# Kernel optimization log

Measured on AMD Instinct MI355X. Metric: run time of the kernel, lower is better.

The kernel has to match this reference:

```python
import jax, jax.numpy as jnp
import numpy as np
from jax import lax

# ---- geometry constants ----
H = W = 128            # image shape
A = 96                 # num angles
D = 128                # detector count
T = 182                # ray integration steps (~128*sqrt(2))
N_ITER = 10
OP_NORM = 128.0

_angles = np.linspace(0.0, np.pi, A, endpoint=False).astype(np.float32)
COS = jnp.asarray(np.cos(_angles))
SIN = jnp.asarray(np.sin(_angles))


def _bilinear(img, xi, yi):
    # img: [B,H,W]; xi,yi: [A,D,T] pixel coords -> [B,A,D,T]
    x0 = jnp.floor(xi)
    y0 = jnp.floor(yi)
    wx = xi - x0
    wy = yi - y0
    x0i = x0.astype(jnp.int32)
    y0i = y0.astype(jnp.int32)
    x1i = x0i + 1
    y1i = y0i + 1

    def g(yy, xx):
        valid = ((xx >= 0) & (xx < W) & (yy >= 0) & (yy < H)).astype(img.dtype)
        v = img[:, jnp.clip(yy, 0, H - 1), jnp.clip(xx, 0, W - 1)]
        return v * valid[None]

    return (g(y0i, x0i) * ((1 - wy) * (1 - wx))[None]
            + g(y0i, x1i) * ((1 - wy) * wx)[None]
            + g(y1i, x0i) * (wy * (1 - wx))[None]
            + g(y1i, x1i) * (wy * wx)[None])


def radon_fwd(x):
    # x: [B,H,W,1] -> sinogram [B,A,D,1]
    img = x[..., 0]
    s = (jnp.arange(D, dtype=jnp.float32) - (D - 1) / 2)[None, :, None]   # [1,D,1]
    t = (jnp.arange(T, dtype=jnp.float32) - (T - 1) / 2)[None, None, :]   # [1,1,T]
    c = COS[:, None, None]
    sn = SIN[:, None, None]
    px = s * c - t * sn            # [A,D,T] world coords
    py = s * sn + t * c
    xi = px + (W - 1) / 2
    yi = py + (H - 1) / 2
    sino = _bilinear(img, xi, yi).sum(axis=-1)   # [B,A,D]
    return sino[..., None]


def radon_adj(sino):
    # sino: [B,A,D,1] -> backprojection [B,H,W,1]
    s = sino[..., 0]   # [B,A,D]
    px = jnp.arange(W, dtype=jnp.float32) - (W - 1) / 2
    py = jnp.arange(H, dtype=jnp.float32) - (H - 1) / 2
    det = (px[None, None, :] * COS[:, None, None]
           + py[None, :, None] * SIN[:, None, None] + (D - 1) / 2)  # [A,H,W]
    d0f = jnp.floor(det)
    w = det - d0f
    d0 = d0f.astype(jnp.int32)
    d1 = d0 + 1
    aidx = jnp.arange(A)[:, None, None]

    def g(dd):
        valid = ((dd >= 0) & (dd < D)).astype(s.dtype)
        return s[:, aidx, jnp.clip(dd, 0, D - 1)] * valid[None]

    out = (g(d0) * (1 - w)[None] + g(d1) * w[None]).sum(axis=1)  # [B,H,W]
    return out[..., None]


def _conv(x, w, b):
    return lax.conv_general_dilated(x, w, (1, 1), 'SAME',
                                    dimension_numbers=('NHWC', 'HWIO', 'NHWC')) + b


def _block(x, w1, b1, w2, b2, w3, b3):
    x = jax.nn.relu(_conv(x, w1, b1))
    x = jax.nn.relu(_conv(x, w2, b2))
    return _conv(x, w3, b3)


def setup_inputs() -> dict:
    key = jax.random.key(0)
    ks = jax.random.split(key, 8)
    B = 4
    sc = 0.05
    return {
        'y': jax.random.normal(ks[0], (B, A, D, 1), jnp.float32),
        'sigma': jnp.full((1,), 0.5, jnp.float32),
        'tau': jnp.full((1,), 0.5, jnp.float32),
        'theta': jnp.ones((1,), jnp.float32),
        'dw1': jax.random.normal(ks[1], (3, 3, 7, 32), jnp.float32) * sc,
        'db1': jnp.zeros((32,), jnp.float32),
        'dw2': jax.random.normal(ks[2], (3, 3, 32, 32), jnp.float32) * sc,
        'db2': jnp.zeros((32,), jnp.float32),
        'dw3': jax.random.normal(ks[3], (3, 3, 32, 5), jnp.float32) * sc,
        'db3': jnp.zeros((5,), jnp.float32),
        'pw1': jax.random.normal(ks[4], (3, 3, 6, 32), jnp.float32) * sc,
        'pb1': jnp.zeros((32,), jnp.float32),
        'pw2': jax.random.normal(ks[5], (3, 3, 32, 32), jnp.float32) * sc,
        'pb2': jnp.zeros((32,), jnp.float32),
        'pw3': jax.random.normal(ks[6], (3, 3, 32, 5), jnp.float32) * sc,
        'pb3': jnp.zeros((5,), jnp.float32),
    }


def reference(y, sigma, tau, theta, dw1, db1, dw2, db2, dw3, db3,
              pw1, pb1, pw2, pb2, pw3, pb3):
    B = y.shape[0]
    n_primal, n_dual = 5, 5
    primal = jnp.zeros((B, H, W, n_primal), y.dtype)
    primal_bar = jnp.zeros((B, H, W, n_primal), y.dtype)
    dual = jnp.zeros((B, A, D, n_dual), y.dtype)

    def step(carry, _):
        primal, primal_bar, dual = carry
        evalop = radon_fwd(primal_bar[..., 1:2]) / OP_NORM
        dual_in = jnp.concatenate([dual, evalop, y], axis=-1)
        dual = dual + sigma * _block(dual_in, dw1, db1, dw2, db2, dw3, db3)
        evalop_adj = radon_adj(dual[..., 0:1]) / OP_NORM
        primal_in = jnp.concatenate([primal, evalop_adj], axis=-1)
        primal_old = primal
        primal = primal + tau * _block(primal_in, pw1, pb1, pw2, pb2, pw3, pb3)
        primal_bar = primal + theta * (primal - primal_old)
        return (primal, primal_bar, dual), None

    (primal, _, _), _ = lax.scan(step, (primal, primal_bar, dual), None, length=N_ITER)
    return primal[..., 0:1]
```

## Files before the change

### kernel.cpp

```cpp
#include <hip/hip_runtime.h>
#include <math.h>

#define BB 4
#define HHH 128
#define WWW 128
#define AANG 96
#define DDET 128
#define TSTEP 182
#define M_P (BB*HHH*WWW)
#define M_D (BB*AANG*DDET)
#define INV_OPN (1.0f/128.0f)

typedef __bf16 bf16x8 __attribute__((ext_vector_type(8)));
typedef float  f32x4  __attribute__((ext_vector_type(4)));

__device__ __forceinline__ void split_store(__bf16* hi, __bf16* lo, int off, float v) {
    __bf16 h = (__bf16)v;
    hi[off] = h;
    lo[off] = (__bf16)(v - (float)h);
}

template<int CIP, int NCH, int NCOT, int IH>
__device__ __forceinline__ void conv_core(
        const __bf16* __restrict__ Ahi, const __bf16* __restrict__ Alo,
        const __bf16* __restrict__ Whi, const __bf16* __restrict__ Wlo,
        int mtile, f32x4 acc[NCOT])
{
    const int IW = 128;
    const int COP = NCOT * 16;
    int lane = threadIdx.x & 63;
    int n16  = lane & 15;
    int quad = lane >> 4;
    int p0  = mtile * 16;
    int b   = p0 / (IH * IW);
    int rem = p0 - b * (IH * IW);
    int ty  = rem >> 7;
    int tx0 = rem & 127;
    #pragma unroll
    for (int c = 0; c < NCH; ++c) {
        int tap = (CIP == 32) ? c : (c * 4 + quad);
        int dy = tap / 3 - 1;
        int dx = tap % 3 - 1;
        int yy = ty + dy;
        int xx = tx0 + n16 + dx;
        bool valid = (tap < 9) && (yy >= 0) && (yy < IH) && (xx >= 0) && (xx < IW);
        bf16x8 a_h = {};
        bf16x8 a_l = {};
        if (valid) {
            size_t off = (size_t)(b * IH * IW + yy * IW + xx) * CIP
                       + ((CIP == 32) ? (quad * 8) : 0);
            a_h = *(const bf16x8*)(Ahi + off);
            a_l = *(const bf16x8*)(Alo + off);
        }
        #pragma unroll
        for (int ct = 0; ct < NCOT; ++ct) {
            size_t woff = ((size_t)tap * COP + ct * 16 + n16) * CIP
                        + ((CIP == 32) ? (quad * 8) : 0);
            bf16x8 b_h = *(const bf16x8*)(Whi + woff);
            bf16x8 b_l = *(const bf16x8*)(Wlo + woff);
            acc[ct] = __builtin_amdgcn_mfma_f32_16x16x32_bf16(a_h, b_h, acc[ct], 0, 0, 0);
            acc[ct] = __builtin_amdgcn_mfma_f32_16x16x32_bf16(a_h, b_l, acc[ct], 0, 0, 0);
            acc[ct] = __builtin_amdgcn_mfma_f32_16x16x32_bf16(a_l, b_h, acc[ct], 0, 0, 0);
        }
    }
}

template<int CIP, int NCH, int IH>
__global__ __launch_bounds__(256) void conv_ab_k(
        const __bf16* __restrict__ Ahi, const __bf16* __restrict__ Alo,
        const __bf16* __restrict__ Whi, const __bf16* __restrict__ Wlo,
        const float* __restrict__ bias,
        __bf16* __restrict__ Ohi, __bf16* __restrict__ Olo, int Mtiles)
{
    int wid = (blockIdx.x * 256 + threadIdx.x) >> 6;
    if (wid >= Mtiles) return;
    f32x4 acc[2] = {};
    conv_core<CIP, NCH, 2, IH>(Ahi, Alo, Whi, Wlo, wid, acc);
    int lane = threadIdx.x & 63;
    int n16 = lane & 15;
    int quad = lane >> 4;
    #pragma unroll
    for (int ct = 0; ct < 2; ++ct) {
        float bv = bias[ct * 16 + n16];
        #pragma unroll
        for (int r = 0; r < 4; ++r) {
            float v = acc[ct][r] + bv;
            v = fmaxf(v, 0.f);
            int m = wid * 16 + quad * 4 + r;
            split_store(Ohi, Olo, m * 32 + ct * 16 + n16, v);
        }
    }
}

template<int IH>
__global__ __launch_bounds__(256) void conv_c_dual_k(
        const __bf16* __restrict__ Ahi, const __bf16* __restrict__ Alo,
        const __bf16* __restrict__ Whi, const __bf16* __restrict__ Wlo,
        const float* __restrict__ bias, const float* __restrict__ sigma_p,
        float* __restrict__ dual_f, __bf16* __restrict__ cat_hi, __bf16* __restrict__ cat_lo,
        float* __restrict__ dual0, int Mtiles)
{
    int wid = (blockIdx.x * 256 + threadIdx.x) >> 6;
    if (wid >= Mtiles) return;
    f32x4 acc[1] = {};
    conv_core<32, 9, 1, IH>(Ahi, Alo, Whi, Wlo, wid, acc);
    int lane = threadIdx.x & 63;
    int n16 = lane & 15;
    int quad = lane >> 4;
    if (n16 < 5) {
        float sg = *sigma_p;
        float bv = bias[n16];
        #pragma unroll
        for (int r = 0; r < 4; ++r) {
            int m = wid * 16 + quad * 4 + r;
            float v = acc[0][r] + bv;
            float dn = dual_f[m * 5 + n16] + sg * v;
            dual_f[m * 5 + n16] = dn;
            split_store(cat_hi, cat_lo, m * 8 + n16, dn);
            if (n16 == 0) dual0[m] = dn;
        }
    }
}

template<int IH>
__global__ __launch_bounds__(256) void conv_c_prim_k(
        const __bf16* __restrict__ Ahi, const __bf16* __restrict__ Alo,
        const __bf16* __restrict__ Whi, const __bf16* __restrict__ Wlo,
        const float* __restrict__ bias, const float* __restrict__ tau_p,
        const float* __restrict__ theta_p,
        float* __restrict__ primal_f, __bf16* __restrict__ cat_hi, __bf16* __restrict__ cat_lo,
        float* __restrict__ pbar1, int Mtiles)
{
    int wid = (blockIdx.x * 256 + threadIdx.x) >> 6;
    if (wid >= Mtiles) return;
    f32x4 acc[1] = {};
    conv_core<32, 9, 1, IH>(Ahi, Alo, Whi, Wlo, wid, acc);
    int lane = threadIdx.x & 63;
    int n16 = lane & 15;
    int quad = lane >> 4;
    if (n16 < 5) {
        float ta = *tau_p;
        float th = *theta_p;
        float bv = bias[n16];
        #pragma unroll
        for (int r = 0; r < 4; ++r) {
            int m = wid * 16 + quad * 4 + r;
            float v = acc[0][r] + bv;
            float pold = primal_f[m * 5 + n16];
            float pn = pold + ta * v;
            primal_f[m * 5 + n16] = pn;
            split_store(cat_hi, cat_lo, m * 8 + n16, pn);
            if (n16 == 1) pbar1[m] = pn + th * (pn - pold);
        }
    }
}

__global__ __launch_bounds__(256) void radon_fwd_part_k(const float* __restrict__ img,
                                                        float* __restrict__ part)
{
    int idx = blockIdx.x * 256 + threadIdx.x;
    int q = idx / M_D;
    int pix = idx - q * M_D;
    int d = pix & 127;
    int b = pix / (AANG * DDET);
    int a = (pix - b * AANG * DDET) >> 7;
    float ang = (float)((double)a * M_PI / (double)AANG);
    float c = cosf(ang), sn = sinf(ang);
    float s = (float)d - 63.5f;
    float scx = s * c, ssy = s * sn;
    const float* ib = img + b * (HHH * WWW);
    float acc = 0.f;
    int t0 = q * 46;
    int t1 = t0 + 46 < TSTEP ? t0 + 46 : TSTEP;
    for (int tt = t0; tt < t1; ++tt) {
        float t = (float)tt - 90.5f;
        float xi = (scx - t * sn) + 63.5f;
        float yi = (ssy + t * c) + 63.5f;
        float x0f = floorf(xi), y0f = floorf(yi);
        float wx = xi - x0f, wy = yi - y0f;
        int x0 = (int)x0f, y0 = (int)y0f;
        int x1 = x0 + 1, y1 = y0 + 1;
        bool xv0 = (x0 >= 0) & (x0 < WWW);
        bool xv1 = (x1 >= 0) & (x1 < WWW);
        bool yv0 = (y0 >= 0) & (y0 < HHH);
        bool yv1 = (y1 >= 0) & (y1 < HHH);
        float v00 = (yv0 & xv0) ? ib[y0 * WWW + x0] : 0.f;
        float v01 = (yv0 & xv1) ? ib[y0 * WWW + x1] : 0.f;
        float v10 = (yv1 & xv0) ? ib[y1 * WWW + x0] : 0.f;
        float v11 = (yv1 & xv1) ? ib[y1 * WWW + x1] : 0.f;
        acc += v00 * (1.f - wy) * (1.f - wx) + v01 * (1.f - wy) * wx
             + v10 * wy * (1.f - wx) + v11 * wy * wx;
    }
    part[idx] = acc;
}

__global__ __launch_bounds__(256) void fwd_combine_k(const float* __restrict__ part,
                                                     __bf16* __restrict__ cat_hi,
                                                     __bf16* __restrict__ cat_lo)
{
    int pix = blockIdx.x * 256 + threadIdx.x;
    if (pix >= M_D) return;
    float v = (part[pix] + part[M_D + pix] + part[2 * M_D + pix] + part[3 * M_D + pix]) * INV_OPN;
    split_store(cat_hi, cat_lo, pix * 8 + 5, v);
}

__global__ __launch_bounds__(256) void radon_adj_part_k(const float* __restrict__ sino0,
                                                        float* __restrict__ part)
{
    __shared__ float cs[AANG], ss[AANG];
    int tid = threadIdx.x;
    if (tid < AANG) {
        double ang = (double)tid * M_PI / (double)AANG;
        cs[tid] = (float)cos(ang);
        ss[tid] = (float)sin(ang);
    }
    __syncthreads();
    int idx = blockIdx.x * 256 + tid;
    int h = idx >> 16;
    int pix = idx & (M_P - 1);
    int x = pix & 127;
    int yv = (pix >> 7) & 127;
    int b = pix >> 14;
    float px = (float)x - 63.5f;
    float py = (float)yv - 63.5f;
    const float* sb = sino0 + b * (AANG * DDET);
    float acc = 0.f;
    int a0 = h * 48;
    for (int a = a0; a < a0 + 48; ++a) {
        float det = px * cs[a] + py * ss[a] + 63.5f;
        float dh = floorf(det);
        float w = det - dh;
        int d0 = (int)dh;
        int d1 = d0 + 1;
        float v0 = (d0 >= 0 && d0 < DDET) ? sb[a * DDET + d0] : 0.f;
        float v1 = (d1 >= 0 && d1 < DDET) ? sb[a * DDET + d1] : 0.f;
        acc += v0 * (1.f - w) + v1 * w;
    }
    part[idx] = acc;
}

__global__ __launch_bounds__(256) void adj_combine_k(const float* __restrict__ part,
                                                     __bf16* __restrict__ cat_hi,
                                                     __bf16* __restrict__ cat_lo)
{
    int pix = blockIdx.x * 256 + threadIdx.x;
    if (pix >= M_P) return;
    float v = (part[pix] + part[M_P + pix]) * INV_OPN;
    split_store(cat_hi, cat_lo, pix * 8 + 5, v);
}

__global__ __launch_bounds__(256) void y_conv_k(const float* __restrict__ y,
                                                __bf16* __restrict__ cat_hi,
                                                __bf16* __restrict__ cat_lo)
{
    int pix = blockIdx.x * 256 + threadIdx.x;
    if (pix >= M_D) return;
    split_store(cat_hi, cat_lo, pix * 8 + 6, y[pix]);
}

__global__ __launch_bounds__(256) void prep_w_k(
        const float* __restrict__ dw1, const float* __restrict__ dw2, const float* __restrict__ dw3,
        const float* __restrict__ pw1, const float* __restrict__ pw2, const float* __restrict__ pw3,
        __bf16* __restrict__ wT)
{
    __bf16* d1h = wT;            __bf16* d1l = d1h + 3072;
    __bf16* d2h = d1l + 3072;    __bf16* d2l = d2h + 9216;
    __bf16* d3h = d2l + 9216;    __bf16* d3l = d3h + 4608;
    __bf16* p1h = d3l + 4608;    __bf16* p1l = p1h + 3072;
    __bf16* p2h = p1l + 3072;    __bf16* p2l = p2h + 9216;
    __bf16* p3h = p2l + 9216;    __bf16* p3l = p3h + 4608;
    int i = blockIdx.x * 256 + threadIdx.x;
    if (i < 2016) {
        int co = i & 31; int r = i >> 5; int ci = r % 7; int tap = r / 7;
        split_store(d1h, d1l, (tap * 32 + co) * 8 + ci, dw1[i]);
        return;
    }
    i -= 2016;
    if (i < 9216) {
        int co = i & 31; int r = i >> 5; int ci = r & 31; int tap = r >> 5;
        split_store(d2h, d2l, (tap * 32 + co) * 32 + ci, dw2[i]);
        return;
    }
    i -= 9216;
    if (i < 1440) {
        int co = i % 5; int r = i / 5; int ci = r & 31; int tap = r >> 5;
        split_store(d3h, d3l, (tap * 16 + co) * 32 + ci, dw3[i]);
        return;
    }
    i -= 1440;
    if (i < 1728) {
        int co = i & 31; int r = i >> 5; int ci = r % 6; int tap = r / 6;
        split_store(p1h, p1l, (tap * 32 + co) * 8 + ci, pw1[i]);
        return;
    }
    i -= 1728;
    if (i < 9216) {
        int co = i & 31; int r = i >> 5; int ci = r & 31; int tap = r >> 5;
        split_store(p2h, p2l, (tap * 32 + co) * 32 + ci, pw2[i]);
        return;
    }
    i -= 9216;
    if (i < 1440) {
        int co = i % 5; int r = i / 5; int ci = r & 31; int tap = r >> 5;
        split_store(p3h, p3l, (tap * 16 + co) * 32 + ci, pw3[i]);
        return;
    }
}

__global__ __launch_bounds__(256) void extract_k(const float* __restrict__ primal_f,
                                                 float* __restrict__ out)
{
    int pix = blockIdx.x * 256 + threadIdx.x;
    if (pix >= M_P) return;
    out[pix] = primal_f[pix * 5];
}

extern "C" void kernel_launch(void* const* d_in, const int* in_sizes, int n_in,
                              void* d_out, int out_size, void* d_ws, size_t ws_size,
                              hipStream_t stream) {
    const float* y     = (const float*)d_in[0];
    const float* sigma = (const float*)d_in[1];
    const float* tau   = (const float*)d_in[2];
    const float* theta = (const float*)d_in[3];
    const float* dw1 = (const float*)d_in[4];
    const float* db1 = (const float*)d_in[5];
    const float* dw2 = (const float*)d_in[6];
    const float* db2 = (const float*)d_in[7];
    const float* dw3 = (const float*)d_in[8];
    const float* db3 = (const float*)d_in[9];
    const float* pw1 = (const float*)d_in[10];
    const float* pb1 = (const float*)d_in[11];
    const float* pw2 = (const float*)d_in[12];
    const float* pb2 = (const float*)d_in[13];
    const float* pw3 = (const float*)d_in[14];
    const float* pb3 = (const float*)d_in[15];

    float* ws = (float*)d_ws;
    float* primal_f = ws;
    float* dual_f   = primal_f + M_P * 5;
    float* pbar1    = dual_f + M_D * 5;
    float* dual0    = pbar1 + M_P;
    float* fwd_part = dual0 + M_D;
    float* adj_part = fwd_part + 4 * M_D;
    __bf16* bf = (__bf16*)(adj_part + 2 * M_P);
    __bf16* cat_d_hi = bf;
    __bf16* cat_d_lo = cat_d_hi + M_D * 8;
    __bf16* cat_p_hi = cat_d_lo + M_D * 8;
    __bf16* cat_p_lo = cat_p_hi + M_P * 8;
    __bf16* hidA_hi  = cat_p_lo + M_P * 8;
    __bf16* hidA_lo  = hidA_hi + M_P * 32;
    __bf16* hidB_hi  = hidA_lo + M_P * 32;
    __bf16* hidB_lo  = hidB_hi + M_P * 32;
    __bf16* wT       = hidB_lo + M_P * 32;

    __bf16* d1h = wT;            __bf16* d1l = d1h + 3072;
    __bf16* d2h = d1l + 3072;    __bf16* d2l = d2h + 9216;
    __bf16* d3h = d2l + 9216;    __bf16* d3l = d3h + 4608;
    __bf16* p1h = d3l + 4608;    __bf16* p1l = p1h + 3072;
    __bf16* p2h = p1l + 3072;    __bf16* p2l = p2h + 9216;
    __bf16* p3h = p2l + 9216;    __bf16* p3l = p3h + 4608;

    hipMemsetAsync(primal_f, 0, (size_t)(M_P * 5 + M_D * 5 + M_P) * 4, stream);
    hipMemsetAsync(cat_d_hi, 0, (size_t)(M_D * 16 + M_P * 16) * 2, stream);
    hipMemsetAsync(wT, 0, (size_t)67584 * 2, stream);

    prep_w_k<<<98, 256, 0, stream>>>(dw1, dw2, dw3, pw1, pw2, pw3, wT);
    y_conv_k<<<M_D / 256, 256, 0, stream>>>(y, cat_d_hi, cat_d_lo);

    const int MT_D = M_D / 16;
    const int MT_P = M_P / 16;

    for (int it = 0; it < 10; ++it) {
        radon_fwd_part_k<<<4 * M_D / 256, 256, 0, stream>>>(pbar1, fwd_part);
        fwd_combine_k<<<M_D / 256, 256, 0, stream>>>(fwd_part, cat_d_hi, cat_d_lo);
        conv_ab_k<8, 3, AANG><<<MT_D / 4, 256, 0, stream>>>(cat_d_hi, cat_d_lo, d1h, d1l, db1, hidA_hi, hidA_lo, MT_D);
        conv_ab_k<32, 9, AANG><<<MT_D / 4, 256, 0, stream>>>(hidA_hi, hidA_lo, d2h, d2l, db2, hidB_hi, hidB_lo, MT_D);
        conv_c_dual_k<AANG><<<MT_D / 4, 256, 0, stream>>>(hidB_hi, hidB_lo, d3h, d3l, db3, sigma, dual_f, cat_d_hi, cat_d_lo, dual0, MT_D);
        radon_adj_part_k<<<2 * M_P / 256, 256, 0, stream>>>(dual0, adj_part);
        adj_combine_k<<<M_P / 256, 256, 0, stream>>>(adj_part, cat_p_hi, cat_p_lo);
        conv_ab_k<8, 3, HHH><<<MT_P / 4, 256, 0, stream>>>(cat_p_hi, cat_p_lo, p1h, p1l, pb1, hidA_hi, hidA_lo, MT_P);
        conv_ab_k<32, 9, HHH><<<MT_P / 4, 256, 0, stream>>>(hidA_hi, hidA_lo, p2h, p2l, pb2, hidB_hi, hidB_lo, MT_P);
        conv_c_prim_k<HHH><<<MT_P / 4, 256, 0, stream>>>(hidB_hi, hidB_lo, p3h, p3l, pb3, tau, theta, primal_f, cat_p_hi, cat_p_lo, pbar1, MT_P);
    }
    extract_k<<<M_P / 256, 256, 0, stream>>>(primal_f, (float*)d_out);
}
```

Measured before the change: 1.168 ms.

## Fuse radon partial sums with combine, clip ray range, precompute trig table

Result: faster. 1.087 ms (-7.0%).

```diff
diff --git a/kernel.cpp b/kernel.cpp
--- a/kernel.cpp
+++ b/kernel.cpp
@@ -155,27 +155,50 @@
     }
 }
 
-__global__ __launch_bounds__(256) void radon_fwd_part_k(const float* __restrict__ img,
-                                                        float* __restrict__ part)
-{
-    int idx = blockIdx.x * 256 + threadIdx.x;
-    int q = idx / M_D;
-    int pix = idx - q * M_D;
+__global__ __launch_bounds__(256) void radon_fwd_fused_k(const float* __restrict__ img,
+                                                         const float* __restrict__ trig,
+                                                         __bf16* __restrict__ cat_hi,
+                                                         __bf16* __restrict__ cat_lo)
+{
+    __shared__ float red[256];
+    int tid = threadIdx.x;
+    int q = tid >> 6;
+    int j = tid & 63;
+    int pix = blockIdx.x * 64 + j;
     int d = pix & 127;
     int b = pix / (AANG * DDET);
     int a = (pix - b * AANG * DDET) >> 7;
-    float ang = (float)((double)a * M_PI / (double)AANG);
-    float c = cosf(ang), sn = sinf(ang);
+    float c  = trig[a];
+    float sn = trig[AANG + a];
     float s = (float)d - 63.5f;
-    float scx = s * c, ssy = s * sn;
+    float A = s * c + 63.5f;
+    float C = s * sn + 63.5f;
+    float tlo = -1e30f, thi = 1e30f;
+    if (sn > 1e-6f) {
+        tlo = (A - 128.f) / sn;
+        thi = (A + 1.f) / sn;
+    }
+    if (c > 1e-6f) {
+        tlo = fmaxf(tlo, (-1.f - C) / c);
+        thi = fminf(thi, (128.f - C) / c);
+    } else if (c < -1e-6f) {
+        tlo = fmaxf(tlo, (128.f - C) / c);
+        thi = fminf(thi, (-1.f - C) / c);
+    }
+    float flo = fmaxf(fminf(tlo + 90.5f, 300.f), -300.f);
+    float fhi = fmaxf(fminf(thi + 90.5f, 300.f), -300.f);
+    int clo = (int)floorf(flo) - 1;
+    int chi = (int)floorf(fhi) + 2;
+    int t0 = q * 46;
+    int t1 = t0 + 46 < TSTEP ? t0 + 46 : TSTEP;
+    if (clo > t0) t0 = clo;
+    if (chi < t1) t1 = chi;
     const float* ib = img + b * (HHH * WWW);
     float acc = 0.f;
-    int t0 = q * 46;
-    int t1 = t0 + 46 < TSTEP ? t0 + 46 : TSTEP;
     for (int tt = t0; tt < t1; ++tt) {
         float t = (float)tt - 90.5f;
-        float xi = (scx - t * sn) + 63.5f;
-        float yi = (ssy + t * c) + 63.5f;
+        float xi = A - t * sn;
+        float yi = C + t * c;
         float x0f = floorf(xi), y0f = floorf(yi);
         float wx = xi - x0f, wy = yi - y0f;
         int x0 = (int)x0f, y0 = (int)y0f;
@@ -191,33 +214,31 @@
         acc += v00 * (1.f - wy) * (1.f - wx) + v01 * (1.f - wy) * wx
              + v10 * wy * (1.f - wx) + v11 * wy * wx;
     }
-    part[idx] = acc;
-}
-
-__global__ __launch_bounds__(256) void fwd_combine_k(const float* __restrict__ part,
-                                                     __bf16* __restrict__ cat_hi,
-                                                     __bf16* __restrict__ cat_lo)
-{
-    int pix = blockIdx.x * 256 + threadIdx.x;
-    if (pix >= M_D) return;
-    float v = (part[pix] + part[M_D + pix] + part[2 * M_D + pix] + part[3 * M_D + pix]) * INV_OPN;
-    split_store(cat_hi, cat_lo, pix * 8 + 5, v);
-}
-
-__global__ __launch_bounds__(256) void radon_adj_part_k(const float* __restrict__ sino0,
-                                                        float* __restrict__ part)
+    red[tid] = acc;
+    __syncthreads();
+    if (tid < 64) {
+        int p2 = blockIdx.x * 64 + tid;
+        float v = (red[tid] + red[tid + 64] + red[tid + 128] + red[tid + 192]) * INV_OPN;
+        split_store(cat_hi, cat_lo, p2 * 8 + 5, v);
+    }
+}
+
+__global__ __launch_bounds__(256) void radon_adj_fused_k(const float* __restrict__ sino0,
+                                                         const float* __restrict__ trig,
+                                                         __bf16* __restrict__ cat_hi,
+                                                         __bf16* __restrict__ cat_lo)
 {
     __shared__ float cs[AANG], ss[AANG];
+    __shared__ float red[256];
     int tid = threadIdx.x;
     if (tid < AANG) {
-        double ang = (double)tid * M_PI / (double)AANG;
-        cs[tid] = (float)cos(ang);
-        ss[tid] = (float)sin(ang);
+        cs[tid] = trig[tid];
+        ss[tid] = trig[AANG + tid];
     }
     __syncthreads();
-    int idx = blockIdx.x * 256 + tid;
-    int h = idx >> 16;
-    int pix = idx & (M_P - 1);
+    int h = tid >> 7;
+    int j = tid & 127;
+    int pix = blockIdx.x * 128 + j;
     int x = pix & 127;
     int yv = (pix >> 7) & 127;
     int b = pix >> 14;
@@ -236,32 +257,20 @@
         float v1 = (d1 >= 0 && d1 < DDET) ? sb[a * DDET + d1] : 0.f;
         acc += v0 * (1.f - w) + v1 * w;
     }
-    part[idx] = acc;
-}
-
-__global__ __launch_bounds__(256) void adj_combine_k(const float* __restrict__ part,
-                                                     __bf16* __restrict__ cat_hi,
-                                                     __bf16* __restrict__ cat_lo)
-{
-    int pix = blockIdx.x * 256 + threadIdx.x;
-    if (pix >= M_P) return;
-    float v = (part[pix] + part[M_P + pix]) * INV_OPN;
-    split_store(cat_hi, cat_lo, pix * 8 + 5, v);
-}
-
-__global__ __launch_bounds__(256) void y_conv_k(const float* __restrict__ y,
-                                                __bf16* __restrict__ cat_hi,
-                                                __bf16* __restrict__ cat_lo)
-{
-    int pix = blockIdx.x * 256 + threadIdx.x;
-    if (pix >= M_D) return;
-    split_store(cat_hi, cat_lo, pix * 8 + 6, y[pix]);
-}
-
-__global__ __launch_bounds__(256) void prep_w_k(
+    red[tid] = acc;
+    __syncthreads();
+    if (tid < 128) {
+        float v = (red[tid] + red[tid + 128]) * INV_OPN;
+        split_store(cat_hi, cat_lo, (blockIdx.x * 128 + tid) * 8 + 5, v);
+    }
+}
+
+__global__ __launch_bounds__(256) void prep_all_k(
         const float* __restrict__ dw1, const float* __restrict__ dw2, const float* __restrict__ dw3,
         const float* __restrict__ pw1, const float* __restrict__ pw2, const float* __restrict__ pw3,
-        __bf16* __restrict__ wT)
+        const float* __restrict__ y,
+        __bf16* __restrict__ wT, float* __restrict__ trig,
+        __bf16* __restrict__ cat_d_hi, __bf16* __restrict__ cat_d_lo)
 {
     __bf16* d1h = wT;            __bf16* d1l = d1h + 3072;
     __bf16* d2h = d1l + 3072;    __bf16* d2l = d2h + 9216;
@@ -270,6 +279,13 @@
     __bf16* p2h = p1l + 3072;    __bf16* p2l = p2h + 9216;
     __bf16* p3h = p2l + 9216;    __bf16* p3l = p3h + 4608;
     int i = blockIdx.x * 256 + threadIdx.x;
+    if (i < AANG) {
+        double ang = (double)i * M_PI / (double)AANG;
+        trig[i] = (float)cos(ang);
+        trig[AANG + i] = (float)sin(ang);
+        return;
+    }
+    i -= AANG;
     if (i < 2016) {
         int co = i & 31; int r = i >> 5; int ci = r % 7; int tap = r / 7;
         split_store(d1h, d1l, (tap * 32 + co) * 8 + ci, dw1[i]);
@@ -303,6 +319,11 @@
     if (i < 1440) {
         int co = i % 5; int r = i / 5; int ci = r & 31; int tap = r >> 5;
         split_store(p3h, p3l, (tap * 16 + co) * 32 + ci, pw3[i]);
+        return;
+    }
+    i -= 1440;
+    if (i < M_D) {
+        split_store(cat_d_hi, cat_d_lo, i * 8 + 6, y[i]);
         return;
     }
 }
@@ -339,19 +360,18 @@
     float* primal_f = ws;
     float* dual_f   = primal_f + M_P * 5;
     float* pbar1    = dual_f + M_D * 5;
-    float* dual0    = pbar1 + M_P;
-    float* fwd_part = dual0 + M_D;
-    float* adj_part = fwd_part + 4 * M_D;
-    __bf16* bf = (__bf16*)(adj_part + 2 * M_P);
+    __bf16* bf = (__bf16*)(pbar1 + M_P);
     __bf16* cat_d_hi = bf;
     __bf16* cat_d_lo = cat_d_hi + M_D * 8;
     __bf16* cat_p_hi = cat_d_lo + M_D * 8;
     __bf16* cat_p_lo = cat_p_hi + M_P * 8;
-    __bf16* hidA_hi  = cat_p_lo + M_P * 8;
-    __bf16* hidA_lo  = hidA_hi + M_P * 32;
-    __bf16* hidB_hi  = hidA_lo + M_P * 32;
-    __bf16* hidB_lo  = hidB_hi + M_P * 32;
-    __bf16* wT       = hidB_lo + M_P * 32;
+    __bf16* wT       = cat_p_lo + M_P * 8;
+    float* trig     = (float*)(wT + 67584);
+    float* dual0    = trig + 192;
+    __bf16* hidA_hi = (__bf16*)(dual0 + M_D);
+    __bf16* hidA_lo = hidA_hi + M_P * 32;
+    __bf16* hidB_hi = hidA_lo + M_P * 32;
+    __bf16* hidB_lo = hidB_hi + M_P * 32;
 
     __bf16* d1h = wT;            __bf16* d1l = d1h + 3072;
     __bf16* d2h = d1l + 3072;    __bf16* d2l = d2h + 9216;
@@ -360,24 +380,25 @@
     __bf16* p2h = p1l + 3072;    __bf16* p2l = p2h + 9216;
     __bf16* p3h = p2l + 9216;    __bf16* p3l = p3h + 4608;
 
-    hipMemsetAsync(primal_f, 0, (size_t)(M_P * 5 + M_D * 5 + M_P) * 4, stream);
-    hipMemsetAsync(cat_d_hi, 0, (size_t)(M_D * 16 + M_P * 16) * 2, stream);
-    hipMemsetAsync(wT, 0, (size_t)67584 * 2, stream);
-
-    prep_w_k<<<98, 256, 0, stream>>>(dw1, dw2, dw3, pw1, pw2, pw3, wT);
-    y_conv_k<<<M_D / 256, 256, 0, stream>>>(y, cat_d_hi, cat_d_lo);
+    size_t zbytes = (size_t)(M_P * 5 + M_D * 5 + M_P) * 4
+                  + (size_t)(M_D * 16 + M_P * 16 + 67584) * 2;
+    hipMemsetAsync(ws, 0, zbytes, stream);
+
+    {
+        int items = AANG + 25056 + M_D;
+        prep_all_k<<<(items + 255) / 256, 256, 0, stream>>>(dw1, dw2, dw3, pw1, pw2, pw3, y,
+                                                            wT, trig, cat_d_hi, cat_d_lo);
+    }
 
     const int MT_D = M_D / 16;
     const int MT_P = M_P / 16;
 
     for (int it = 0; it < 10; ++it) {
-        radon_fwd_part_k<<<4 * M_D / 256, 256, 0, stream>>>(pbar1, fwd_part);
-        fwd_combine_k<<<M_D / 256, 256, 0, stream>>>(fwd_part, cat_d_hi, cat_d_lo);
+        radon_fwd_fused_k<<<M_D / 64, 256, 0, stream>>>(pbar1, trig, cat_d_hi, cat_d_lo);
         conv_ab_k<8, 3, AANG><<<MT_D / 4, 256, 0, stream>>>(cat_d_hi, cat_d_lo, d1h, d1l, db1, hidA_hi, hidA_lo, MT_D);
         conv_ab_k<32, 9, AANG><<<MT_D / 4, 256, 0, stream>>>(hidA_hi, hidA_lo, d2h, d2l, db2, hidB_hi, hidB_lo, MT_D);
         conv_c_dual_k<AANG><<<MT_D / 4, 256, 0, stream>>>(hidB_hi, hidB_lo, d3h, d3l, db3, sigma, dual_f, cat_d_hi, cat_d_lo, dual0, MT_D);
-        radon_adj_part_k<<<2 * M_P / 256, 256, 0, stream>>>(dual0, adj_part);
-        adj_combine_k<<<M_P / 256, 256, 0, stream>>>(adj_part, cat_p_hi, cat_p_lo);
+        radon_adj_fused_k<<<M_P / 128, 256, 0, stream>>>(dual0, trig, cat_p_hi, cat_p_lo);
         conv_ab_k<8, 3, HHH><<<MT_P / 4, 256, 0, stream>>>(cat_p_hi, cat_p_lo, p1h, p1l, pb1, hidA_hi, hidA_lo, MT_P);
         conv_ab_k<32, 9, HHH><<<MT_P / 4, 256, 0, stream>>>(hidA_hi, hidA_lo, p2h, p2l, pb2, hidB_hi, hidB_lo, MT_P);
         conv_c_prim_k<HHH><<<MT_P / 4, 256, 0, stream>>>(hidB_hi, hidB_lo, p3h, p3l, pb3, tau, theta, primal_f, cat_p_hi, cat_p_lo, pbar1, MT_P);
```
